# Kernel tuning notes

Hardware: AMD Instinct MI355X
Metric: run time of the kernel (lower is better)

## Reference

```python
import jax, jax.numpy as jnp
import numpy as np

L, B = 1024, 64
VALID_FRAC = 0.9  # fraction of residues with nonzero (observed) coordinates in y


def setup_inputs() -> dict:
    key = jax.random.key(0)
    kx, ky = jax.random.split(key)
    x = jax.random.normal(kx, (L, B, 3), dtype=jnp.float32)
    y = jax.random.normal(ky, (L, B, 3), dtype=jnp.float32)
    # zero out trailing residues in y so the dynamic mask (co.sum() != 0) is exercised
    valid = (jnp.arange(L) < int(VALID_FRAC * L))[:, None, None]
    y = y * valid.astype(jnp.float32)
    return {"x": x, "y": y}


def _masked_pair_dist(pts, pair_mask):
    # pts: [B, L, 3]; pair_mask: [B, L, L] (False on diagonal and on padded rows/cols)
    sq = jnp.sum(pts * pts, axis=-1)                                   # [B, L]
    d2 = sq[:, :, None] + sq[:, None, :] - 2.0 * jnp.einsum('bld,bmd->blm', pts, pts)
    d2 = jnp.maximum(d2, 0.0)                                          # relu, matches F.relu
    safe = jnp.where(pair_mask, d2, 1.0)                               # keep sqrt grad finite
    return jnp.where(pair_mask, jnp.sqrt(safe), 0.0)


def reference(x, y):
    # x, y: [L, B, 3] -> permute to [B, L, 3] as in the torch module
    xb = jnp.transpose(x, (1, 0, 2))
    yb = jnp.transpose(y, (1, 0, 2))
    Bn, Ln = xb.shape[0], xb.shape[1]
    # mask: residues of y whose coordinate sum is nonzero (index_select in original)
    mask = (jnp.sum(yb, axis=-1) != 0)                                 # [B, L]
    off_diag = ~jnp.eye(Ln, dtype=bool)
    pair_mask = mask[:, :, None] & mask[:, None, :] & off_diag         # [B, L, L]
    xd = _masked_pair_dist(xb, pair_mask)
    yd = _masked_pair_dist(yb, pair_mask)
    D = yd - xd                                                        # [B, L, L]
    per_batch = jnp.sqrt(jnp.sum(D * D, axis=(1, 2)))                  # Frobenius norm per batch
    denom = (Ln ** 2 / 2 - Ln) ** 0.5                                  # x.size(1)**2/2 - x.size(1)
    out = jnp.sum(per_batch) / denom / Bn
    return out.reshape(1)
```

## Files before the change

kernel.cpp:

```cpp
#include <hip/hip_runtime.h>
#include <math.h>

#define Lp 1024
#define Bp 64
#define Tt 128
#define NTILE 8
#define NPAIR 36

__global__ __launch_bounds__(256) void drmsd_main(
    const float* __restrict__ x, const float* __restrict__ y,
    float* __restrict__ partials)
{
    __shared__ float4 xs[2][Tt];
    __shared__ float4 ys[2][Tt];
    __shared__ float  red[4];

    const int b = blockIdx.x;
    const int p = blockIdx.y;

    int ti = 0, base = 0;
    while (p >= base + (NTILE - ti)) { base += (NTILE - ti); ++ti; }
    const int tj = ti + (p - base);

    const int t = threadIdx.x;

    {
        const int r     = t & (Tt - 1);
        const int which = t >> 7;
        const int tile  = which ? tj : ti;
        const int row   = tile * Tt + r;
        const float* px = x + (size_t)row * (Bp * 3) + (size_t)b * 3;
        const float* py = y + (size_t)row * (Bp * 3) + (size_t)b * 3;
        const float x0 = px[0], x1 = px[1], x2 = px[2];
        const float y0 = py[0], y1 = py[1], y2 = py[2];
        const float m  = ((y0 + y1 + y2) != 0.0f) ? 1.0f : 0.0f;
        xs[which][r] = make_float4(x0, x1, x2, 0.0f);
        ys[which][r] = make_float4(y0, y1, y2, m);
    }
    __syncthreads();

    const int jslice = t & 15;
    const int rg     = t >> 4;
    float total = 0.0f;

#pragma unroll
    for (int ii = 0; ii < 2; ++ii) {
        const int i0 = ii * 64 + rg * 4;
        float4 xi[4], yi[4];
        float  acc[4];
#pragma unroll
        for (int r = 0; r < 4; ++r) {
            xi[r]  = xs[0][i0 + r];
            yi[r]  = ys[0][i0 + r];
            acc[r] = 0.0f;
        }
#pragma unroll
        for (int jj = 0; jj < 8; ++jj) {
            const int j = jj * 16 + jslice;
            const float4 xj = xs[1][j];
            const float4 yj = ys[1][j];
#pragma unroll
            for (int r = 0; r < 4; ++r) {
                const float ax = xi[r].x - xj.x;
                const float ay = xi[r].y - xj.y;
                const float az = xi[r].z - xj.z;
                const float d2x = ax * ax + ay * ay + az * az;
                const float dx  = __builtin_amdgcn_sqrtf(d2x);
                const float bx = yi[r].x - yj.x;
                const float by = yi[r].y - yj.y;
                const float bz = yi[r].z - yj.z;
                const float d2y = bx * bx + by * by + bz * bz;
                const float dy  = __builtin_amdgcn_sqrtf(d2y);
                const float dm  = (dy - dx) * yj.w;
                acc[r] = fmaf(dm, dm, acc[r]);
            }
        }
#pragma unroll
        for (int r = 0; r < 4; ++r) total = fmaf(acc[r], yi[r].w, total);
    }

#pragma unroll
    for (int off = 32; off > 0; off >>= 1)
        total += __shfl_down(total, off, 64);
    const int wave = t >> 6;
    if ((t & 63) == 0) red[wave] = total;
    __syncthreads();
    if (t == 0) {
        float s = red[0] + red[1] + red[2] + red[3];
        if (ti != tj) s *= 2.0f;
        partials[(size_t)b * NPAIR + p] = s;
    }
}

__global__ __launch_bounds__(64) void drmsd_final(
    const float* __restrict__ partials, float* __restrict__ out)
{
    const int b = threadIdx.x;
    float s = 0.0f;
#pragma unroll
    for (int pidx = 0; pidx < NPAIR; ++pidx)
        s += partials[(size_t)b * NPAIR + pidx];
    float pb = sqrtf(s);
#pragma unroll
    for (int off = 32; off > 0; off >>= 1)
        pb += __shfl_down(pb, off, 64);
    if (b == 0) {
        const double denom = sqrt((double)Lp * (double)Lp / 2.0 - (double)Lp);
        out[0] = (float)((double)pb / denom / (double)Bp);
    }
}

extern "C" void kernel_launch(void* const* d_in, const int* in_sizes, int n_in,
                              void* d_out, int out_size, void* d_ws, size_t ws_size,
                              hipStream_t stream) {
    const float* x = (const float*)d_in[0];
    const float* y = (const float*)d_in[1];
    float* out      = (float*)d_out;
    float* partials = (float*)d_ws;

    dim3 grid(Bp, NPAIR);
    drmsd_main<<<grid, 256, 0, stream>>>(x, y, partials);
    drmsd_final<<<1, 64, 0, stream>>>(partials, out);
}
```

Baseline: 76.07 us.

## Use one sqrt per pair via algebraic expansion and SoA shared layout

Rewrites (sqrt(dy2)-sqrt(dx2))^2 as dx2+dy2-2*sqrt(dx2*dy2), so each pair needs one square root instead of two. Shared memory changes from packed float4 records to separate per-coordinate arrays, with float4/float2 vector loads, and each thread handles two adjacent j columns per iteration. This cuts transcendental throughput pressure, at the cost of possible cancellation error when the two distances are close and a larger product range inside the sqrt.

```diff
diff --git a/kernel.cpp b/kernel.cpp
--- a/kernel.cpp
+++ b/kernel.cpp
@@ -11,9 +11,10 @@
     const float* __restrict__ x, const float* __restrict__ y,
     float* __restrict__ partials)
 {
-    __shared__ float4 xs[2][Tt];
-    __shared__ float4 ys[2][Tt];
-    __shared__ float  red[4];
+    __shared__ __align__(16) float xsx[2][Tt], xsy[2][Tt], xsz[2][Tt];
+    __shared__ __align__(16) float ysx[2][Tt], ysy[2][Tt], ysz[2][Tt];
+    __shared__ __align__(16) float ms[2][Tt];
+    __shared__ float red[4];
 
     const int b = blockIdx.x;
     const int p = blockIdx.y;
@@ -33,50 +34,77 @@
         const float* py = y + (size_t)row * (Bp * 3) + (size_t)b * 3;
         const float x0 = px[0], x1 = px[1], x2 = px[2];
         const float y0 = py[0], y1 = py[1], y2 = py[2];
-        const float m  = ((y0 + y1 + y2) != 0.0f) ? 1.0f : 0.0f;
-        xs[which][r] = make_float4(x0, x1, x2, 0.0f);
-        ys[which][r] = make_float4(y0, y1, y2, m);
+        xsx[which][r] = x0; xsy[which][r] = x1; xsz[which][r] = x2;
+        ysx[which][r] = y0; ysy[which][r] = y1; ysz[which][r] = y2;
+        ms[which][r]  = ((y0 + y1 + y2) != 0.0f) ? 1.0f : 0.0f;
     }
     __syncthreads();
 
-    const int jslice = t & 15;
-    const int rg     = t >> 4;
+    const int jsl2 = (t & 15) << 1;
+    const int rg   = t >> 4;
+
     float total = 0.0f;
 
 #pragma unroll
-    for (int ii = 0; ii < 2; ++ii) {
-        const int i0 = ii * 64 + rg * 4;
-        float4 xi[4], yi[4];
-        float  acc[4];
+    for (int half = 0; half < 2; ++half) {
+        const int i0 = half * 64 + rg * 4;
+        const float4 v_xx = *(const float4*)&xsx[0][i0];
+        const float4 v_xy = *(const float4*)&xsy[0][i0];
+        const float4 v_xz = *(const float4*)&xsz[0][i0];
+        const float4 v_yx = *(const float4*)&ysx[0][i0];
+        const float4 v_yy = *(const float4*)&ysy[0][i0];
+        const float4 v_yz = *(const float4*)&ysz[0][i0];
+        const float4 v_mi = *(const float4*)&ms[0][i0];
+        const float xix[4] = { v_xx.x, v_xx.y, v_xx.z, v_xx.w };
+        const float xiy[4] = { v_xy.x, v_xy.y, v_xy.z, v_xy.w };
+        const float xiz[4] = { v_xz.x, v_xz.y, v_xz.z, v_xz.w };
+        const float yix[4] = { v_yx.x, v_yx.y, v_yx.z, v_yx.w };
+        const float yiy[4] = { v_yy.x, v_yy.y, v_yy.z, v_yy.w };
+        const float yiz[4] = { v_yz.x, v_yz.y, v_yz.z, v_yz.w };
+        const float mir[4] = { v_mi.x, v_mi.y, v_mi.z, v_mi.w };
+
+        float accA[4] = {0.f, 0.f, 0.f, 0.f};
+        float accB[4] = {0.f, 0.f, 0.f, 0.f};
+
 #pragma unroll
-        for (int r = 0; r < 4; ++r) {
-            xi[r]  = xs[0][i0 + r];
-            yi[r]  = ys[0][i0 + r];
-            acc[r] = 0.0f;
-        }
-#pragma unroll
-        for (int jj = 0; jj < 8; ++jj) {
-            const int j = jj * 16 + jslice;
-            const float4 xj = xs[1][j];
-            const float4 yj = ys[1][j];
+        for (int jj = 0; jj < 4; ++jj) {
+            const int j0 = jj * 32 + jsl2;
+            const float2 xjx = *(const float2*)&xsx[1][j0];
+            const float2 xjy = *(const float2*)&xsy[1][j0];
+            const float2 xjz = *(const float2*)&xsz[1][j0];
+            const float2 yjx = *(const float2*)&ysx[1][j0];
+            const float2 yjy = *(const float2*)&ysy[1][j0];
+            const float2 yjz = *(const float2*)&ysz[1][j0];
+            const float2 mj  = *(const float2*)&ms[1][j0];
 #pragma unroll
             for (int r = 0; r < 4; ++r) {
-                const float ax = xi[r].x - xj.x;
-                const float ay = xi[r].y - xj.y;
-                const float az = xi[r].z - xj.z;
-                const float d2x = ax * ax + ay * ay + az * az;
-                const float dx  = __builtin_amdgcn_sqrtf(d2x);
-                const float bx = yi[r].x - yj.x;
-                const float by = yi[r].y - yj.y;
-                const float bz = yi[r].z - yj.z;
-                const float d2y = bx * bx + by * by + bz * bz;
-                const float dy  = __builtin_amdgcn_sqrtf(d2y);
-                const float dm  = (dy - dx) * yj.w;
-                acc[r] = fmaf(dm, dm, acc[r]);
+                const float axA = xix[r] - xjx.x;
+                const float ayA = xiy[r] - xjy.x;
+                const float azA = xiz[r] - xjz.x;
+                const float dxA = fmaf(axA, axA, fmaf(ayA, ayA, azA * azA));
+                const float bxA = yix[r] - yjx.x;
+                const float byA = yiy[r] - yjy.x;
+                const float bzA = yiz[r] - yjz.x;
+                const float dyA = fmaf(bxA, bxA, fmaf(byA, byA, bzA * bzA));
+                const float sA  = __builtin_amdgcn_sqrtf(dxA * dyA);
+                const float uA  = fmaf(-2.0f, sA, dxA + dyA);
+                accA[r] = fmaf(mj.x, uA, accA[r]);
+                const float axB = xix[r] - xjx.y;
+                const float ayB = xiy[r] - xjy.y;
+                const float azB = xiz[r] - xjz.y;
+                const float dxB = fmaf(axB, axB, fmaf(ayB, ayB, azB * azB));
+                const float bxB = yix[r] - yjx.y;
+                const float byB = yiy[r] - yjy.y;
+                const float bzB = yiz[r] - yjz.y;
+                const float dyB = fmaf(bxB, bxB, fmaf(byB, byB, bzB * bzB));
+                const float sB  = __builtin_amdgcn_sqrtf(dxB * dyB);
+                const float uB  = fmaf(-2.0f, sB, dxB + dyB);
+                accB[r] = fmaf(mj.y, uB, accB[r]);
             }
         }
 #pragma unroll
-        for (int r = 0; r < 4; ++r) total = fmaf(acc[r], yi[r].w, total);
+        for (int r = 0; r < 4; ++r)
+            total = fmaf(accA[r] + accB[r], mir[r], total);
     }
 
 #pragma unroll
```

Measured after the change: 75.49 us. No clear change (-0.8%).
